# Performance work log

Measured on AMD Instinct MI355X. Metric: run time of the kernel, lower is better.

Reference implementation:

```python
import jax, jax.numpy as jnp
import numpy as np
from jax.experimental.jet import jet
from jax.experimental.ode import odeint

STATE = 4096
CDIM = 1024
TAY_REG = 2


def sol_recursive(order, f, z, t):
    """Higher-order derivatives of the ODE dynamics via Taylor-mode (jet)."""
    if order < 2:
        return f(z, t), jnp.zeros_like(z)
    z_shape = z.shape
    z_t = jnp.concatenate((jnp.ravel(z), jnp.array([t], dtype=z.dtype)))

    def g(z_t):
        zz, tt = jnp.reshape(z_t[:-1], z_shape), z_t[-1]
        dz = jnp.ravel(f(zz, tt))
        dt = jnp.array([1.0], dtype=z_t.dtype)
        return jnp.concatenate((dz, dt))

    y0, yns = jet(g, (z_t,), ((jnp.ones_like(z_t),),))
    for _ in range(order - 1):
        y0, yns = jet(g, (z_t,), ((y0, *yns),))
    return jnp.reshape(y0[:-1], z_shape), jnp.reshape(yns[-2][:-1], z_shape)


def augment_dynamics(reg, dynamics):
    def aug_dynamics(yr, t):
        y, r = yr
        dydt, dy_r = sol_recursive(reg, dynamics, y, t)
        return dydt, jnp.mean(dy_r ** 2)[None] * jnp.ones(1, y.dtype) if False else (dydt, jnp.mean(dy_r ** 2) * jnp.ones(1, y.dtype))
    # flatten conditional artifact: redefine cleanly
    def aug(yr, t):
        y, r = yr
        dydt, dy_r = sol_recursive(reg, dynamics, y, t)
        return dydt, jnp.mean(dy_r ** 2) * jnp.ones(1, y.dtype)
    return aug


def setup_inputs() -> dict:
    key = jax.random.key(0)
    ks = jax.random.split(key, 5)
    fan_in = CDIM + STATE + 1
    s = 0.5 / np.sqrt(fan_in)  # tame Lipschitz constant -> modest adaptive step count
    h = jax.random.normal(ks[0], (STATE,), dtype=jnp.float32)
    c = jax.random.normal(ks[1], (CDIM,), dtype=jnp.float32)
    t = jnp.float32(1.0)
    W1 = jax.random.normal(ks[2], (fan_in, STATE), dtype=jnp.float32) * s
    b1 = jnp.zeros((STATE,), dtype=jnp.float32)
    W2 = jax.random.normal(ks[3], (fan_in, STATE), dtype=jnp.float32) * s
    b2 = jnp.zeros((STATE,), dtype=jnp.float32)
    return {"h": h, "t": t, "c": c, "W1": W1, "b1": b1, "W2": W2, "b2": b2}


def reference(h, t, c, W1, b1, W2, b2):
    # MLPDynamics: sigmoid(h) -> hstack(c, ., t) -> lin1 -> sigmoid -> hstack(c, ., t) -> lin2
    def dyn(hh, tt):
        out = jax.nn.sigmoid(hh)
        x = jnp.hstack((c, out, tt))          # [CDIM+STATE+1]
        out = jax.nn.sigmoid(x @ W1 + b1)     # [STATE]
        x2 = jnp.hstack((c, out, tt))
        return x2 @ W2 + b2                   # [STATE]

    aug = augment_dynamics(TAY_REG, dyn)
    ts = jnp.stack([jnp.zeros_like(t), t])
    ys, rs = odeint(aug, (h, jnp.zeros(1, h.dtype)), ts)
    # jnp.split(., 2)[1].squeeze() over the 2-row time axis == take row 1
    h1 = ys[1]
    r1 = rs[1].squeeze()
    return (h1, r1)
```

## Files before the change

### kernel.cpp

```cpp
#include <hip/hip_runtime.h>

#define N      4096
#define NC     1024
#define STEPS  4
#define TPB    256
#define NBLK   512

typedef unsigned short us8 __attribute__((ext_vector_type(8)));

__device__ __forceinline__ float bf2f(unsigned short u) {
  union { unsigned int i; float f; } v; v.i = ((unsigned int)u) << 16; return v.f;
}
__device__ __forceinline__ unsigned short f2bf(float f) {
  union { float f; unsigned int i; } v; v.f = f;
  const unsigned int u = v.i;
  return (unsigned short)((u + 0x7FFFu + ((u >> 16) & 1u)) >> 16);
}
__device__ __forceinline__ float sigf(float x) { return 1.0f / (1.0f + __expf(-x)); }

__global__ __launch_bounds__(TPB) void k_init(const float* __restrict__ h,
                                              const float* __restrict__ W1,
                                              const float* __restrict__ W2,
                                              const float* __restrict__ b1,
                                              const float* __restrict__ b2,
                                              float* __restrict__ ycur,
                                              float* __restrict__ cp1,
                                              float* __restrict__ cp2,
                                              float* __restrict__ xA,
                                              float* __restrict__ T1,
                                              float* __restrict__ T2,
                                              float* __restrict__ rk) {
  const int j = blockIdx.x * TPB + threadIdx.x;
  if (j < N) {
    ycur[j] = h[j];
    cp1[j] = b1[j];
    cp2[j] = b2[j];
    xA[j] = sigf(h[j]);
    T1[j] = W1[(size_t)(NC + N) * N + j];
    T2[j] = W2[(size_t)(NC + N) * N + j];
  }
  if (j < 16) rk[j] = 0.f;
}

__global__ __launch_bounds__(TPB) void k_conv(const float* __restrict__ W1,
                                              const float* __restrict__ W2,
                                              unsigned short* __restrict__ Wt1,
                                              unsigned short* __restrict__ Wt2) {
  __shared__ float tile[64][65];
  const float* __restrict__ W = blockIdx.z ? W2 : W1;
  unsigned short* __restrict__ Wt = blockIdx.z ? Wt2 : Wt1;
  const int i0 = blockIdx.x * 64;
  const int j0 = blockIdx.y * 64;
  const int c = threadIdx.x & 63, rq = threadIdx.x >> 6;
#pragma unroll
  for (int m = 0; m < 16; ++m) {
    const int ii = (m << 2) + rq;
    tile[ii][c] = W[(size_t)(NC + i0 + ii) * N + j0 + c];
  }
  __syncthreads();
#pragma unroll
  for (int m = 0; m < 16; ++m) {
    const int jj = (m << 2) + rq;
    Wt[(size_t)(j0 + jj) * N + i0 + c] = f2bf(tile[c][jj]);
  }
}

__global__ __launch_bounds__(TPB) void k_cpart(const float* __restrict__ W1,
                                               const float* __restrict__ W2,
                                               const float* __restrict__ c,
                                               float* __restrict__ cp1,
                                               float* __restrict__ cp2) {
  const float* __restrict__ W = blockIdx.z ? W2 : W1;
  float* __restrict__ cp = blockIdx.z ? cp2 : cp1;
  __shared__ float xs[128];
  __shared__ float red[8][256];
  const int tid = threadIdx.x;
  const int cb = blockIdx.x, rc = blockIdx.y;
  const int r0 = rc * 128;
  if (tid < 128) xs[tid] = c[r0 + tid];
  __syncthreads();
  const int cg = tid & 31, rg = tid >> 5;
  const float* __restrict__ wbase = W + (size_t)r0 * N + cb * 256 + cg * 8;
  float a[8] = {0,0,0,0,0,0,0,0};
#pragma unroll
  for (int k = 0; k < 16; ++k) {
    const int r = rg + (k << 3);
    const float xv = xs[r];
    const float4 wa = *reinterpret_cast<const float4*>(wbase + (size_t)r * N);
    const float4 wb = *reinterpret_cast<const float4*>(wbase + (size_t)r * N + 4);
    a[0] = fmaf(wa.x, xv, a[0]); a[1] = fmaf(wa.y, xv, a[1]);
    a[2] = fmaf(wa.z, xv, a[2]); a[3] = fmaf(wa.w, xv, a[3]);
    a[4] = fmaf(wb.x, xv, a[4]); a[5] = fmaf(wb.y, xv, a[5]);
    a[6] = fmaf(wb.z, xv, a[6]); a[7] = fmaf(wb.w, xv, a[7]);
  }
#pragma unroll
  for (int e = 0; e < 8; ++e) red[rg][cg * 8 + e] = a[e];
  __syncthreads();
  float ssum = 0.f;
#pragma unroll
  for (int g = 0; g < 8; ++g) ssum += red[g][tid];
  atomicAdd(&cp[cb * 256 + tid], ssum);
}

__global__ __launch_bounds__(TPB) void k_phase(
    int mode,
    const unsigned short* __restrict__ Wt,
    const float* __restrict__ T,
    const float* __restrict__ cp,
    const float* __restrict__ xin,
    float* __restrict__ xout,
    float* __restrict__ fbuf,
    const float* __restrict__ tptr,
    float* __restrict__ ycur,
    float* __restrict__ ksum,
    float* __restrict__ rk,
    int rkIdx, int s, float csvn, float tA, float tB) {
  __shared__ float xs[N];
  __shared__ float red[4];
  const int tid = threadIdx.x;
#pragma unroll
  for (int q = 0; q < 4; ++q)
    reinterpret_cast<float4*>(xs)[q * 256 + tid] =
        reinterpret_cast<const float4*>(xin)[q * 256 + tid];
  __syncthreads();

  const int w = tid >> 6, l = tid & 63;
  const int j0 = blockIdx.x * 8 + w * 2;
  const unsigned short* __restrict__ w0 = Wt + (size_t)j0 * N;
  const unsigned short* __restrict__ w1 = w0 + N;
  float a0 = 0.f, a1 = 0.f;
#pragma unroll
  for (int p = 0; p < 8; ++p) {
    const int off = (p << 9) + (l << 3);
    const us8 wa = *reinterpret_cast<const us8*>(w0 + off);
    const us8 wb = *reinterpret_cast<const us8*>(w1 + off);
    const float* xp = xs + off;
#pragma unroll
    for (int e = 0; e < 8; ++e) {
      a0 = fmaf(bf2f(wa[e]), xp[e], a0);
      a1 = fmaf(bf2f(wb[e]), xp[e], a1);
    }
  }
#pragma unroll
  for (int o = 32; o >= 1; o >>= 1) {
    a0 += __shfl_down(a0, o);
    a1 += __shfl_down(a1, o);
  }

  if (l == 0) {
    const float dt = tptr[0] * (1.0f / STEPS);
    const float tcoef = fmaf(tA, dt, tB);
    float v = 0.f;
    float dots[2] = {a0, a1};
#pragma unroll
    for (int e = 0; e < 2; ++e) {
      const int j = j0 + e;
      const float a = fmaf(tcoef, T[j], dots[e]);
      if (mode == 0) {
        xout[j] = sigf(a + cp[j]);
      } else if (mode == 1) {
        const float fv = a + cp[j];
        fbuf[j] = fv;
        const float s0 = xout[j];
        xout[j] = s0 * (1.f - s0) * fv;
      } else if (mode == 2) {
        const float s1 = xout[j];
        xout[j] = s1 * (1.f - s1) * a;
      } else {
        v += a * a;
        const float fc = fbuf[j];
        float y = ycur[j];
        if (s == 0)      ksum[j] = fc;
        else if (s < 3)  ksum[j] = fmaf(2.f, fc, ksum[j]);
        else { y = fmaf(dt * (1.f / 6.f), ksum[j] + fc, y); ycur[j] = y; }
        xout[j] = sigf(fmaf(csvn * dt, fc, y));
      }
    }
    if (mode == 3) red[w] = v;
  }
  if (mode == 3) {
    __syncthreads();
    if (tid == 0) atomicAdd(&rk[rkIdx], red[0] + red[1] + red[2] + red[3]);
  }
}

__global__ __launch_bounds__(128) void k_fin(const float* __restrict__ ycur,
                                             float* __restrict__ out) {
  const int j = blockIdx.x * 128 + threadIdx.x;
  out[j] = ycur[j];
}

__global__ void k_out(const float* __restrict__ rk, const float* __restrict__ tptr,
                      float* __restrict__ out) {
  if (threadIdx.x == 0) {
    const float dt = tptr[0] * (1.0f / STEPS);
    float r = 0.f;
    for (int st = 0; st < STEPS; ++st)
      r += rk[4 * st] + 2.f * rk[4 * st + 1] + 2.f * rk[4 * st + 2] + rk[4 * st + 3];
    out[N] = r * (dt / 6.f) * (1.0f / N);
  }
}

extern "C" void kernel_launch(void* const* d_in, const int* in_sizes, int n_in,
                              void* d_out, int out_size, void* d_ws, size_t ws_size,
                              hipStream_t stream) {
  const float* h  = (const float*)d_in[0];
  const float* t  = (const float*)d_in[1];
  const float* c  = (const float*)d_in[2];
  const float* W1 = (const float*)d_in[3];
  const float* b1 = (const float*)d_in[4];
  const float* W2 = (const float*)d_in[5];
  const float* b2 = (const float*)d_in[6];
  float* out = (float*)d_out;

  char* ws = (char*)d_ws;
  const size_t wb = (size_t)N * N * sizeof(unsigned short);
  unsigned short* Wt1 = (unsigned short*)ws;
  unsigned short* Wt2 = (unsigned short*)(ws + wb);
  float* fp = (float*)(ws + 2 * wb);
  float* xA   = fp;
  float* xB   = xA + N;
  float* cp1  = xB + N;
  float* cp2  = cp1 + N;
  float* fbuf = cp2 + N;
  float* ycur = fbuf + N;
  float* ksum = ycur + N;
  float* T1   = ksum + N;
  float* T2   = T1 + N;
  float* rk   = T2 + N;

  k_init<<<16, TPB, 0, stream>>>(h, W1, W2, b1, b2, ycur, cp1, cp2, xA, T1, T2, rk);
  k_conv<<<dim3(64, 64, 2), TPB, 0, stream>>>(W1, W2, Wt1, Wt2);
  k_cpart<<<dim3(16, 8, 2), TPB, 0, stream>>>(W1, W2, c, cp1, cp2);

  const float csv[4] = {0.f, 0.5f, 0.5f, 1.f};
  float* xb[2] = {xA, xB};
  int xp = 0;
  for (int i = 0; i < 16; ++i) {
    const int step = i >> 2, s = i & 3;
    const float tsv = (float)step + csv[s];
    k_phase<<<NBLK, TPB, 0, stream>>>(0, Wt1, T1, cp1, xb[xp], xb[xp ^ 1], fbuf,
                                      t, ycur, ksum, rk, 0, s, 0.f, tsv, 0.f);
    xp ^= 1;
    k_phase<<<NBLK, TPB, 0, stream>>>(1, Wt2, T2, cp2, xb[xp], xb[xp ^ 1], fbuf,
                                      t, ycur, ksum, rk, 0, s, 0.f, tsv, 0.f);
    xp ^= 1;
    k_phase<<<NBLK, TPB, 0, stream>>>(2, Wt1, T1, nullptr, xb[xp], xb[xp ^ 1], fbuf,
                                      t, ycur, ksum, rk, 0, s, 0.f, 0.f, 1.f);
    xp ^= 1;
    k_phase<<<NBLK, TPB, 0, stream>>>(3, Wt2, T2, nullptr, xb[xp], xb[xp ^ 1], fbuf,
                                      t, ycur, ksum, rk, i, s, csv[(s + 1) & 3],
                                      0.f, 1.f);
    xp ^= 1;
  }
  k_fin<<<32, 128, 0, stream>>>(ycur, out);
  k_out<<<1, 64, 0, stream>>>(rk, t, out);
}
```

Before: 863.2 us.

## Stream weight rows into LDS via direct global-to-LDS loads, keep x in registers

```diff
diff --git a/kernel.cpp b/kernel.cpp
--- a/kernel.cpp
+++ b/kernel.cpp
@@ -4,7 +4,6 @@
 #define NC     1024
 #define STEPS  4
 #define TPB    256
-#define NBLK   512
 
 typedef unsigned short us8 __attribute__((ext_vector_type(8)));
 
@@ -17,6 +16,13 @@
   return (unsigned short)((u + 0x7FFFu + ((u >> 16) & 1u)) >> 16);
 }
 __device__ __forceinline__ float sigf(float x) { return 1.0f / (1.0f + __expf(-x)); }
+
+__device__ __forceinline__ void load16(const unsigned short* g, unsigned short* l) {
+  __builtin_amdgcn_global_load_lds(
+      (__attribute__((address_space(1))) void*)(g),
+      (__attribute__((address_space(3))) void*)(l),
+      16, 0, 0);
+}
 
 __global__ __launch_bounds__(TPB) void k_init(const float* __restrict__ h,
                                               const float* __restrict__ W1,
@@ -59,9 +65,13 @@
   }
   __syncthreads();
 #pragma unroll
-  for (int m = 0; m < 16; ++m) {
-    const int jj = (m << 2) + rq;
-    Wt[(size_t)(j0 + jj) * N + i0 + c] = f2bf(tile[c][jj]);
+  for (int it = 0; it < 2; ++it) {
+    const int lin = it * 256 + threadIdx.x;
+    const int jj = lin >> 3, g = lin & 7;
+    us8 o;
+#pragma unroll
+    for (int e = 0; e < 8; ++e) o[e] = f2bf(tile[g * 8 + e][jj]);
+    *reinterpret_cast<us8*>(&Wt[(size_t)(j0 + jj) * N + i0 + g * 8]) = o;
   }
 }
 
@@ -115,84 +125,92 @@
     float* __restrict__ ksum,
     float* __restrict__ rk,
     int rkIdx, int s, float csvn, float tA, float tB) {
-  __shared__ float xs[N];
-  __shared__ float red[4];
+  __shared__ unsigned short wlds[4][4096];
+  __shared__ float red2[16];
   const int tid = threadIdx.x;
-#pragma unroll
-  for (int q = 0; q < 4; ++q)
-    reinterpret_cast<float4*>(xs)[q * 256 + tid] =
-        reinterpret_cast<const float4*>(xin)[q * 256 + tid];
-  __syncthreads();
-
   const int w = tid >> 6, l = tid & 63;
-  const int j0 = blockIdx.x * 8 + w * 2;
-  const unsigned short* __restrict__ w0 = Wt + (size_t)j0 * N;
-  const unsigned short* __restrict__ w1 = w0 + N;
-  float a0 = 0.f, a1 = 0.f;
-#pragma unroll
-  for (int p = 0; p < 8; ++p) {
-    const int off = (p << 9) + (l << 3);
-    const us8 wa = *reinterpret_cast<const us8*>(w0 + off);
-    const us8 wb = *reinterpret_cast<const us8*>(w1 + off);
-    const float* xp = xs + off;
-#pragma unroll
-    for (int e = 0; e < 8; ++e) {
-      a0 = fmaf(bf2f(wa[e]), xp[e], a0);
-      a1 = fmaf(bf2f(wb[e]), xp[e], a1);
+  const int j0 = blockIdx.x * 4;
+  const int rbase = (w << 10) + (l << 3);
+
+#pragma unroll
+  for (int cc = 0; cc < 4; ++cc) {
+#pragma unroll
+    for (int k = 0; k < 2; ++k) {
+      const unsigned short* g =
+          Wt + ((size_t)(j0 + cc) << 12) + (w << 10) + (k << 9) + (l << 3);
+      load16(g, &wlds[cc][(w << 10) + (k << 9)]);
     }
   }
-#pragma unroll
-  for (int o = 32; o >= 1; o >>= 1) {
-    a0 += __shfl_down(a0, o);
-    a1 += __shfl_down(a1, o);
-  }
-
+  float xa[2][8];
+#pragma unroll
+  for (int p = 0; p < 2; ++p) {
+    const float4 a = *reinterpret_cast<const float4*>(xin + rbase + (p << 9));
+    const float4 b = *reinterpret_cast<const float4*>(xin + rbase + (p << 9) + 4);
+    xa[p][0] = a.x; xa[p][1] = a.y; xa[p][2] = a.z; xa[p][3] = a.w;
+    xa[p][4] = b.x; xa[p][5] = b.y; xa[p][6] = b.z; xa[p][7] = b.w;
+  }
+  __syncthreads();
+
+  float acc[4] = {0.f, 0.f, 0.f, 0.f};
+#pragma unroll
+  for (int cc = 0; cc < 4; ++cc) {
+#pragma unroll
+    for (int p = 0; p < 2; ++p) {
+      const us8 wv = *reinterpret_cast<const us8*>(&wlds[cc][rbase + (p << 9)]);
+#pragma unroll
+      for (int e = 0; e < 8; ++e)
+        acc[cc] = fmaf(bf2f(wv[e]), xa[p][e], acc[cc]);
+    }
+  }
+#pragma unroll
+  for (int cc = 0; cc < 4; ++cc) {
+#pragma unroll
+    for (int o = 32; o >= 1; o >>= 1) acc[cc] += __shfl_down(acc[cc], o);
+  }
   if (l == 0) {
+#pragma unroll
+    for (int cc = 0; cc < 4; ++cc) red2[w * 4 + cc] = acc[cc];
+  }
+  __syncthreads();
+
+  if (tid < 4) {
+    const int j = j0 + tid;
+    const float dot = red2[tid] + red2[4 + tid] + red2[8 + tid] + red2[12 + tid];
     const float dt = tptr[0] * (1.0f / STEPS);
     const float tcoef = fmaf(tA, dt, tB);
-    float v = 0.f;
-    float dots[2] = {a0, a1};
-#pragma unroll
-    for (int e = 0; e < 2; ++e) {
-      const int j = j0 + e;
-      const float a = fmaf(tcoef, T[j], dots[e]);
-      if (mode == 0) {
-        xout[j] = sigf(a + cp[j]);
-      } else if (mode == 1) {
-        const float fv = a + cp[j];
-        fbuf[j] = fv;
-        const float s0 = xout[j];
-        xout[j] = s0 * (1.f - s0) * fv;
-      } else if (mode == 2) {
-        const float s1 = xout[j];
-        xout[j] = s1 * (1.f - s1) * a;
-      } else {
-        v += a * a;
-        const float fc = fbuf[j];
-        float y = ycur[j];
-        if (s == 0)      ksum[j] = fc;
-        else if (s < 3)  ksum[j] = fmaf(2.f, fc, ksum[j]);
-        else { y = fmaf(dt * (1.f / 6.f), ksum[j] + fc, y); ycur[j] = y; }
-        xout[j] = sigf(fmaf(csvn * dt, fc, y));
-      }
+    const float a = fmaf(tcoef, T[j], dot);
+    if (mode == 0) {
+      xout[j] = sigf(a + cp[j]);
+    } else if (mode == 1) {
+      const float fv = a + cp[j];
+      fbuf[j] = fv;
+      const float s0 = xout[j];
+      xout[j] = s0 * (1.f - s0) * fv;
+    } else if (mode == 2) {
+      const float s1 = xout[j];
+      xout[j] = s1 * (1.f - s1) * a;
+    } else {
+      float v = a * a;
+      const float fc = fbuf[j];
+      float y = ycur[j];
+      if (s == 0)      ksum[j] = fc;
+      else if (s < 3)  ksum[j] = fmaf(2.f, fc, ksum[j]);
+      else { y = fmaf(dt * (1.f / 6.f), ksum[j] + fc, y); ycur[j] = y; }
+      xout[j] = sigf(fmaf(csvn * dt, fc, y));
+      v += __shfl_down(v, 2);
+      v += __shfl_down(v, 1);
+      if (tid == 0) atomicAdd(&rk[rkIdx], v);
     }
-    if (mode == 3) red[w] = v;
-  }
-  if (mode == 3) {
-    __syncthreads();
-    if (tid == 0) atomicAdd(&rk[rkIdx], red[0] + red[1] + red[2] + red[3]);
   }
 }
 
 __global__ __launch_bounds__(128) void k_fin(const float* __restrict__ ycur,
+                                             const float* __restrict__ rk,
+                                             const float* __restrict__ tptr,
                                              float* __restrict__ out) {
   const int j = blockIdx.x * 128 + threadIdx.x;
-  out[j] = ycur[j];
-}
-
-__global__ void k_out(const float* __restrict__ rk, const float* __restrict__ tptr,
-                      float* __restrict__ out) {
-  if (threadIdx.x == 0) {
+  if (j < N) out[j] = ycur[j];
+  if (j == 0) {
     const float dt = tptr[0] * (1.0f / STEPS);
     float r = 0.f;
     for (int st = 0; st < STEPS; ++st)
@@ -239,20 +257,19 @@
   for (int i = 0; i < 16; ++i) {
     const int step = i >> 2, s = i & 3;
     const float tsv = (float)step + csv[s];
-    k_phase<<<NBLK, TPB, 0, stream>>>(0, Wt1, T1, cp1, xb[xp], xb[xp ^ 1], fbuf,
+    k_phase<<<1024, TPB, 0, stream>>>(0, Wt1, T1, cp1, xb[xp], xb[xp ^ 1], fbuf,
                                       t, ycur, ksum, rk, 0, s, 0.f, tsv, 0.f);
     xp ^= 1;
-    k_phase<<<NBLK, TPB, 0, stream>>>(1, Wt2, T2, cp2, xb[xp], xb[xp ^ 1], fbuf,
+    k_phase<<<1024, TPB, 0, stream>>>(1, Wt2, T2, cp2, xb[xp], xb[xp ^ 1], fbuf,
                                       t, ycur, ksum, rk, 0, s, 0.f, tsv, 0.f);
     xp ^= 1;
-    k_phase<<<NBLK, TPB, 0, stream>>>(2, Wt1, T1, nullptr, xb[xp], xb[xp ^ 1], fbuf,
+    k_phase<<<1024, TPB, 0, stream>>>(2, Wt1, T1, nullptr, xb[xp], xb[xp ^ 1], fbuf,
                                       t, ycur, ksum, rk, 0, s, 0.f, 0.f, 1.f);
     xp ^= 1;
-    k_phase<<<NBLK, TPB, 0, stream>>>(3, Wt2, T2, nullptr, xb[xp], xb[xp ^ 1], fbuf,
+    k_phase<<<1024, TPB, 0, stream>>>(3, Wt2, T2, nullptr, xb[xp], xb[xp ^ 1], fbuf,
                                       t, ycur, ksum, rk, i, s, csv[(s + 1) & 3],
                                       0.f, 1.f);
     xp ^= 1;
   }
-  k_fin<<<32, 128, 0, stream>>>(ycur, out);
-  k_out<<<1, 64, 0, stream>>>(rk, t, out);
-}
+  k_fin<<<32, 128, 0, stream>>>(ycur, rk, t, out);
+}
```

Measured after the change: 885.0 us. 2.5% more time.
